# Performance work log

Hardware: AMD Instinct MI355X
Metric: run time of the kernel (lower is better)

## Reference

```python
import jax, jax.numpy as jnp
import numpy as np

B, S = 8192, 2048
EPS = 1e-8
DISCOUNT_FACTOR = 0.99
AVERAGE_LAMBDA = 0.9


def setup_inputs() -> dict:
    key = jax.random.key(0)
    k1, k2 = jax.random.split(key)
    values = jax.random.normal(k1, (B, S + 1, 1), dtype=jnp.float32)
    rewards = jax.random.normal(k2, (B, S, 1), dtype=jnp.float32)
    dones = jnp.zeros((B, S, 1), dtype=jnp.float32)
    # parameters initialized as in the module: atanh of target values
    raw_gamma = jnp.arctanh(jnp.full((1,), DISCOUNT_FACTOR, dtype=jnp.float32))
    raw_lambd = jnp.arctanh(jnp.full((S,), AVERAGE_LAMBDA, dtype=jnp.float32))
    return {"values": values, "rewards": rewards, "dones": dones,
            "raw_gamma": raw_gamma, "raw_lambd": raw_lambd}


def reference(values, rewards, dones, raw_gamma, raw_lambd):
    # gamma = tanh(raw_gamma).clamp_min(1e-8); lambda likewise (per timestep)
    gamma = jnp.maximum(jnp.tanh(raw_gamma), EPS)      # [1]
    lam = jnp.maximum(jnp.tanh(raw_lambd), EPS)        # [S]
    # time-major for scan: [S, B, 1]
    v_next = jnp.swapaxes(values[:, 1:], 0, 1)
    r = jnp.swapaxes(rewards, 0, 1)
    d = jnp.swapaxes(dones, 0, 1)

    def step(G, xs):
        vt1, rt, dt, lt = xs
        # G_t = r_t + gamma*(1-d_t)*((1-lam_t)*V_{t+1} + lam_t*G_{t+1})
        G = rt + gamma * (1.0 - dt) * ((1.0 - lt) * vt1 + lt * G)
        return G, G

    G_last = values[:, -1]  # bootstrap: [B, 1]
    _, Gs = jax.lax.scan(step, G_last, (v_next, r, d, lam), reverse=True)
    return jnp.swapaxes(Gs, 0, 1)  # [B, S, 1]
```

## Files before the change

kernel.cpp:

```cpp
#include <hip/hip_runtime.h>
#include <math.h>

#define EPS_F 1e-8f

__global__ void lam_prep_kernel(const float* __restrict__ raw_lambd,
                                float* __restrict__ lam_ws, int S) {
    int t = blockIdx.x * blockDim.x + threadIdx.x;
    if (t < S) lam_ws[t] = fmaxf(tanhf(raw_lambd[t]), EPS_F);
}

template <bool USE_WS>
__global__ __launch_bounds__(256) void glam_scan_kernel(
    const float* __restrict__ values,
    const float* __restrict__ rewards,
    const float* __restrict__ dones,
    const float* __restrict__ raw_gamma,
    const float* __restrict__ raw_lambd,
    const float* __restrict__ lam_ws,
    float* __restrict__ out,
    int B, int S)
{
    const int wave = (blockIdx.x * blockDim.x + threadIdx.x) >> 6;
    const int lane = threadIdx.x & 63;
    if (wave >= B) return;

    const float gamma = fmaxf(tanhf(raw_gamma[0]), EPS_F);

    const size_t vbase = (size_t)wave * (size_t)(S + 1);
    const size_t base  = (size_t)wave * (size_t)S;

    const int NP = S >> 8;
    float carry = values[vbase + S];

    #pragma unroll 8
    for (int p = NP - 1; p >= 0; --p) {
        const int c0 = p << 8;
        const int e0 = c0 + 4 * lane;

        const float4 r4 = *reinterpret_cast<const float4*>(rewards + base + e0);
        const float4 d4 = *reinterpret_cast<const float4*>(dones   + base + e0);

        float lamv[4];
        if (USE_WS) {
            const float4 l4 = *reinterpret_cast<const float4*>(lam_ws + e0);
            lamv[0] = l4.x; lamv[1] = l4.y; lamv[2] = l4.z; lamv[3] = l4.w;
        } else {
            #pragma unroll
            for (int j = 0; j < 4; ++j)
                lamv[j] = fmaxf(tanhf(raw_lambd[e0 + j]), EPS_F);
        }

        float v1[4];
        #pragma unroll
        for (int j = 0; j < 4; ++j) v1[j] = values[vbase + e0 + j + 1];

        const float rr[4] = { r4.x, r4.y, r4.z, r4.w };
        const float dd[4] = { d4.x, d4.y, d4.z, d4.w };

        float a[4], bb[4];
        #pragma unroll
        for (int j = 0; j < 4; ++j) {
            const float c = gamma * (1.0f - dd[j]);
            a[j]  = fmaf(c * (1.0f - lamv[j]), v1[j], rr[j]);
            bb[j] = c * lamv[j];
        }

        float A = 0.0f, P = 1.0f;
        #pragma unroll
        for (int j = 3; j >= 0; --j) {
            A = fmaf(bb[j], A, a[j]);
            P *= bb[j];
        }

        #pragma unroll
        for (int d = 1; d < 64; d <<= 1) {
            float A2 = __shfl_down(A, d);
            float P2 = __shfl_down(P, d);
            const bool valid = (lane + d) < 64;
            A2 = valid ? A2 : 0.0f;
            P2 = valid ? P2 : 1.0f;
            A = fmaf(P, A2, A);
            P *= P2;
        }

        const float A1 = __shfl_down(A, 1);
        const float P1 = __shfl_down(P, 1);
        float G = (lane == 63) ? carry : fmaf(P1, carry, A1);

        float o[4];
        #pragma unroll
        for (int j = 3; j >= 0; --j) {
            G = fmaf(bb[j], G, a[j]);
            o[j] = G;
        }

        float4 o4;
        o4.x = o[0]; o4.y = o[1]; o4.z = o[2]; o4.w = o[3];
        *reinterpret_cast<float4*>(out + base + e0) = o4;

        carry = __shfl(G, 0);
    }
}

__global__ void glam_naive_kernel(const float* __restrict__ values,
                                  const float* __restrict__ rewards,
                                  const float* __restrict__ dones,
                                  const float* __restrict__ raw_gamma,
                                  const float* __restrict__ raw_lambd,
                                  float* __restrict__ out, int B, int S) {
    int b = blockIdx.x * blockDim.x + threadIdx.x;
    if (b >= B) return;
    const float gamma = fmaxf(tanhf(raw_gamma[0]), EPS_F);
    const size_t vbase = (size_t)b * (size_t)(S + 1);
    const size_t base  = (size_t)b * (size_t)S;
    float G = values[vbase + S];
    for (int t = S - 1; t >= 0; --t) {
        const float lt = fmaxf(tanhf(raw_lambd[t]), EPS_F);
        const float c  = gamma * (1.0f - dones[base + t]);
        G = rewards[base + t] + c * ((1.0f - lt) * values[vbase + t + 1] + lt * G);
        out[base + t] = G;
    }
}

extern "C" void kernel_launch(void* const* d_in, const int* in_sizes, int n_in,
                              void* d_out, int out_size, void* d_ws, size_t ws_size,
                              hipStream_t stream) {
    const float* values    = (const float*)d_in[0];
    const float* rewards   = (const float*)d_in[1];
    const float* dones     = (const float*)d_in[2];
    const float* raw_gamma = (const float*)d_in[3];
    const float* raw_lambd = (const float*)d_in[4];
    float* out = (float*)d_out;

    const int S = in_sizes[4];
    const int B = in_sizes[1] / S;

    if ((S & 255) != 0) {
        glam_naive_kernel<<<(B + 255) / 256, 256, 0, stream>>>(
            values, rewards, dones, raw_gamma, raw_lambd, out, B, S);
        return;
    }

    const int total_threads = B * 64;
    const int blocks = (total_threads + 255) / 256;

    const bool use_ws = (d_ws != nullptr) && (ws_size >= (size_t)S * sizeof(float));
    if (use_ws) {
        float* lam_ws = (float*)d_ws;
        lam_prep_kernel<<<(S + 255) / 256, 256, 0, stream>>>(raw_lambd, lam_ws, S);
        glam_scan_kernel<true><<<blocks, 256, 0, stream>>>(
            values, rewards, dones, raw_gamma, raw_lambd, lam_ws, out, B, S);
    } else {
        glam_scan_kernel<false><<<blocks, 256, 0, stream>>>(
            values, rewards, dones, raw_gamma, raw_lambd, nullptr, out, B, S);
    }
}
```

Measured before the change: 49.80 us.

## Decouple chunk scans from serial carry chain with affine composition and nontemporal stores

Each wave now computes the local affine scan (A, P) for all eight chunks independently and keeps them in registers. A short backward pass then applies the carry to produce the outputs. This takes the cross-chunk carry off the critical path, so the loads and shuffle scans for all chunks can overlap. S is fixed at 2048 as a compile-time constant, and outputs use nontemporal stores. The cost is much higher register pressure from the per-chunk arrays, which may reduce occupancy, and the fast path only handles S=2048.

```diff
diff --git a/kernel.cpp b/kernel.cpp
--- a/kernel.cpp
+++ b/kernel.cpp
@@ -2,6 +2,8 @@
 #include <math.h>
 
 #define EPS_F 1e-8f
+
+typedef float vfloat4 __attribute__((ext_vector_type(4)));
 
 __global__ void lam_prep_kernel(const float* __restrict__ raw_lambd,
                                 float* __restrict__ lam_ws, int S) {
@@ -18,8 +20,11 @@
     const float* __restrict__ raw_lambd,
     const float* __restrict__ lam_ws,
     float* __restrict__ out,
-    int B, int S)
+    int B)
 {
+    constexpr int S  = 2048;
+    constexpr int NP = 8;
+
     const int wave = (blockIdx.x * blockDim.x + threadIdx.x) >> 6;
     const int lane = threadIdx.x & 63;
     if (wave >= B) return;
@@ -28,21 +33,23 @@
 
     const size_t vbase = (size_t)wave * (size_t)(S + 1);
     const size_t base  = (size_t)wave * (size_t)S;
+    const int lo4 = 4 * lane;
 
-    const int NP = S >> 8;
-    float carry = values[vbase + S];
+    const float vS = values[vbase + S];
 
-    #pragma unroll 8
-    for (int p = NP - 1; p >= 0; --p) {
-        const int c0 = p << 8;
-        const int e0 = c0 + 4 * lane;
+    float oA[NP][4], oP[NP][4];
+    float pA[NP], pP[NP];
 
-        const float4 r4 = *reinterpret_cast<const float4*>(rewards + base + e0);
-        const float4 d4 = *reinterpret_cast<const float4*>(dones   + base + e0);
+    #pragma unroll
+    for (int p = 0; p < NP; ++p) {
+        const int e0 = (p << 8) + lo4;
+
+        const vfloat4 r4 = *reinterpret_cast<const vfloat4*>(rewards + base + e0);
+        const vfloat4 d4 = *reinterpret_cast<const vfloat4*>(dones   + base + e0);
 
         float lamv[4];
         if (USE_WS) {
-            const float4 l4 = *reinterpret_cast<const float4*>(lam_ws + e0);
+            const vfloat4 l4 = *reinterpret_cast<const vfloat4*>(lam_ws + e0);
             lamv[0] = l4.x; lamv[1] = l4.y; lamv[2] = l4.z; lamv[3] = l4.w;
         } else {
             #pragma unroll
@@ -52,7 +59,7 @@
 
         float v1[4];
         #pragma unroll
-        for (int j = 0; j < 4; ++j) v1[j] = values[vbase + e0 + j + 1];
+        for (int j = 0; j < 4; ++j) v1[j] = values[vbase + e0 + 1 + j];
 
         const float rr[4] = { r4.x, r4.y, r4.z, r4.w };
         const float dd[4] = { d4.x, d4.y, d4.z, d4.w };
@@ -83,22 +90,34 @@
             P *= P2;
         }
 
+        pA[p] = __shfl(A, 0);
+        pP[p] = __shfl(P, 0);
+
         const float A1 = __shfl_down(A, 1);
         const float P1 = __shfl_down(P, 1);
-        float G = (lane == 63) ? carry : fmaf(P1, carry, A1);
+        float Af = (lane == 63) ? 0.0f : A1;
+        float Pf = (lane == 63) ? 1.0f : P1;
 
-        float o[4];
         #pragma unroll
         for (int j = 3; j >= 0; --j) {
-            G = fmaf(bb[j], G, a[j]);
-            o[j] = G;
+            Af = fmaf(bb[j], Af, a[j]);
+            Pf = bb[j] * Pf;
+            oA[p][j] = Af;
+            oP[p][j] = Pf;
         }
+    }
 
-        float4 o4;
-        o4.x = o[0]; o4.y = o[1]; o4.z = o[2]; o4.w = o[3];
-        *reinterpret_cast<float4*>(out + base + e0) = o4;
-
-        carry = __shfl(G, 0);
+    float Gb = vS;
+    #pragma unroll
+    for (int p = NP - 1; p >= 0; --p) {
+        vfloat4 o4;
+        o4.x = fmaf(oP[p][0], Gb, oA[p][0]);
+        o4.y = fmaf(oP[p][1], Gb, oA[p][1]);
+        o4.z = fmaf(oP[p][2], Gb, oA[p][2]);
+        o4.w = fmaf(oP[p][3], Gb, oA[p][3]);
+        __builtin_nontemporal_store(o4,
+            reinterpret_cast<vfloat4*>(out + base + (p << 8) + lo4));
+        Gb = fmaf(pP[p], Gb, pA[p]);
     }
 }
 
@@ -135,7 +154,7 @@
     const int S = in_sizes[4];
     const int B = in_sizes[1] / S;
 
-    if ((S & 255) != 0) {
+    if (S != 2048) {
         glam_naive_kernel<<<(B + 255) / 256, 256, 0, stream>>>(
             values, rewards, dones, raw_gamma, raw_lambd, out, B, S);
         return;
@@ -149,9 +168,9 @@
         float* lam_ws = (float*)d_ws;
         lam_prep_kernel<<<(S + 255) / 256, 256, 0, stream>>>(raw_lambd, lam_ws, S);
         glam_scan_kernel<true><<<blocks, 256, 0, stream>>>(
-            values, rewards, dones, raw_gamma, raw_lambd, lam_ws, out, B, S);
+            values, rewards, dones, raw_gamma, raw_lambd, lam_ws, out, B);
     } else {
         glam_scan_kernel<false><<<blocks, 256, 0, stream>>>(
-            values, rewards, dones, raw_gamma, raw_lambd, nullptr, out, B, S);
+            values, rewards, dones, raw_gamma, raw_lambd, nullptr, out, B);
     }
 }
```

After: 49.31 us. Within noise of the previous version (-1.0%).

## Scan each row with one 512-thread block using cross-wave LDS carry combine

Applied to the files above, without the earlier changes.

Each batch row is now handled by one 512-thread block of eight waves, each wave covering a 256-element chunk. Previously a single wave walked the eight chunks sequentially with a serial carry between them. Per-wave affine scan summaries are exchanged through shared memory after one barrier, and each wave composes the later summaries to get its carry. This exposes more memory-level parallelism and removes the serial chunk dependency. It also adds a vectorized unaligned load for values, precomputes gamma into the workspace, and uses nontemporal stores. The kernel now hardcodes S=2048 and falls back to the naive path otherwise.

```diff
diff --git a/kernel.cpp b/kernel.cpp
--- a/kernel.cpp
+++ b/kernel.cpp
@@ -3,103 +3,111 @@
 
 #define EPS_F 1e-8f
 
-__global__ void lam_prep_kernel(const float* __restrict__ raw_lambd,
-                                float* __restrict__ lam_ws, int S) {
+typedef float vfloat4 __attribute__((ext_vector_type(4)));
+typedef float uafloat4 __attribute__((ext_vector_type(4), aligned(4)));
+
+__global__ void lam_prep_kernel(const float* __restrict__ raw_gamma,
+                                const float* __restrict__ raw_lambd,
+                                float* __restrict__ ws, int S) {
     int t = blockIdx.x * blockDim.x + threadIdx.x;
-    if (t < S) lam_ws[t] = fmaxf(tanhf(raw_lambd[t]), EPS_F);
+    if (t < S) ws[t] = fmaxf(tanhf(raw_lambd[t]), EPS_F);
+    if (t == S) ws[S] = fmaxf(tanhf(raw_gamma[0]), EPS_F);
 }
 
 template <bool USE_WS>
-__global__ __launch_bounds__(256) void glam_scan_kernel(
+__global__ __launch_bounds__(512, 8) void glam_scan_kernel(
     const float* __restrict__ values,
     const float* __restrict__ rewards,
     const float* __restrict__ dones,
     const float* __restrict__ raw_gamma,
     const float* __restrict__ raw_lambd,
-    const float* __restrict__ lam_ws,
+    const float* __restrict__ ws,
     float* __restrict__ out,
-    int B, int S)
+    int B)
 {
-    const int wave = (blockIdx.x * blockDim.x + threadIdx.x) >> 6;
-    const int lane = threadIdx.x & 63;
-    if (wave >= B) return;
+    constexpr int S = 2048;
 
-    const float gamma = fmaxf(tanhf(raw_gamma[0]), EPS_F);
+    __shared__ float cA[8], cP[8];
 
-    const size_t vbase = (size_t)wave * (size_t)(S + 1);
-    const size_t base  = (size_t)wave * (size_t)S;
+    const int tid  = threadIdx.x;
+    const int w    = tid >> 6;
+    const int lane = tid & 63;
+    const int row  = blockIdx.x;
 
-    const int NP = S >> 8;
-    float carry = values[vbase + S];
+    const size_t vbase = (size_t)row * (size_t)(S + 1);
+    const size_t base  = (size_t)row * (size_t)S;
+    const int e0 = (w << 8) + 4 * lane;
 
-    #pragma unroll 8
-    for (int p = NP - 1; p >= 0; --p) {
-        const int c0 = p << 8;
-        const int e0 = c0 + 4 * lane;
+    const vfloat4  r4 = *reinterpret_cast<const vfloat4*>(rewards + base + e0);
+    const vfloat4  d4 = *reinterpret_cast<const vfloat4*>(dones   + base + e0);
+    const uafloat4 v4 = *reinterpret_cast<const uafloat4*>(values + vbase + e0 + 1);
+    const float    vS = values[vbase + S];
 
-        const float4 r4 = *reinterpret_cast<const float4*>(rewards + base + e0);
-        const float4 d4 = *reinterpret_cast<const float4*>(dones   + base + e0);
+    float gamma, ll[4];
+    if (USE_WS) {
+        const vfloat4 l4 = *reinterpret_cast<const vfloat4*>(ws + e0);
+        ll[0] = l4.x; ll[1] = l4.y; ll[2] = l4.z; ll[3] = l4.w;
+        gamma = ws[S];
+    } else {
+        #pragma unroll
+        for (int j = 0; j < 4; ++j)
+            ll[j] = fmaxf(tanhf(raw_lambd[e0 + j]), EPS_F);
+        gamma = fmaxf(tanhf(raw_gamma[0]), EPS_F);
+    }
 
-        float lamv[4];
-        if (USE_WS) {
-            const float4 l4 = *reinterpret_cast<const float4*>(lam_ws + e0);
-            lamv[0] = l4.x; lamv[1] = l4.y; lamv[2] = l4.z; lamv[3] = l4.w;
-        } else {
-            #pragma unroll
-            for (int j = 0; j < 4; ++j)
-                lamv[j] = fmaxf(tanhf(raw_lambd[e0 + j]), EPS_F);
-        }
+    const float rr[4] = { r4.x, r4.y, r4.z, r4.w };
+    const float dd[4] = { d4.x, d4.y, d4.z, d4.w };
+    const float vv[4] = { v4.x, v4.y, v4.z, v4.w };
 
-        float v1[4];
-        #pragma unroll
-        for (int j = 0; j < 4; ++j) v1[j] = values[vbase + e0 + j + 1];
+    float a[4], bb[4];
+    #pragma unroll
+    for (int j = 0; j < 4; ++j) {
+        const float c = gamma * (1.0f - dd[j]);
+        a[j]  = fmaf(c * (1.0f - ll[j]), vv[j], rr[j]);
+        bb[j] = c * ll[j];
+    }
 
-        const float rr[4] = { r4.x, r4.y, r4.z, r4.w };
-        const float dd[4] = { d4.x, d4.y, d4.z, d4.w };
+    float A = 0.0f, P = 1.0f;
+    #pragma unroll
+    for (int j = 3; j >= 0; --j) {
+        A = fmaf(bb[j], A, a[j]);
+        P *= bb[j];
+    }
 
-        float a[4], bb[4];
-        #pragma unroll
-        for (int j = 0; j < 4; ++j) {
-            const float c = gamma * (1.0f - dd[j]);
-            a[j]  = fmaf(c * (1.0f - lamv[j]), v1[j], rr[j]);
-            bb[j] = c * lamv[j];
-        }
+    #pragma unroll
+    for (int d = 1; d < 64; d <<= 1) {
+        float A2 = __shfl_down(A, d);
+        float P2 = __shfl_down(P, d);
+        const bool valid = (lane + d) < 64;
+        A2 = valid ? A2 : 0.0f;
+        P2 = valid ? P2 : 1.0f;
+        A = fmaf(P, A2, A);
+        P *= P2;
+    }
 
-        float A = 0.0f, P = 1.0f;
-        #pragma unroll
-        for (int j = 3; j >= 0; --j) {
-            A = fmaf(bb[j], A, a[j]);
-            P *= bb[j];
-        }
+    if (lane == 0) { cA[w] = A; cP[w] = P; }
 
-        #pragma unroll
-        for (int d = 1; d < 64; d <<= 1) {
-            float A2 = __shfl_down(A, d);
-            float P2 = __shfl_down(P, d);
-            const bool valid = (lane + d) < 64;
-            A2 = valid ? A2 : 0.0f;
-            P2 = valid ? P2 : 1.0f;
-            A = fmaf(P, A2, A);
-            P *= P2;
-        }
+    const float Ad = __shfl_down(A, 1);
+    const float Pd = __shfl_down(P, 1);
+    const float A1 = (lane == 63) ? 0.0f : Ad;
+    const float P1 = (lane == 63) ? 1.0f : Pd;
 
-        const float A1 = __shfl_down(A, 1);
-        const float P1 = __shfl_down(P, 1);
-        float G = (lane == 63) ? carry : fmaf(P1, carry, A1);
+    __syncthreads();
 
-        float o[4];
-        #pragma unroll
-        for (int j = 3; j >= 0; --j) {
-            G = fmaf(bb[j], G, a[j]);
-            o[j] = G;
-        }
+    float Gb = vS;
+    for (int q = 7; q > w; --q)
+        Gb = fmaf(cP[q], Gb, cA[q]);
 
-        float4 o4;
-        o4.x = o[0]; o4.y = o[1]; o4.z = o[2]; o4.w = o[3];
-        *reinterpret_cast<float4*>(out + base + e0) = o4;
-
-        carry = __shfl(G, 0);
+    float G = fmaf(P1, Gb, A1);
+    float o[4];
+    #pragma unroll
+    for (int j = 3; j >= 0; --j) {
+        G = fmaf(bb[j], G, a[j]);
+        o[j] = G;
     }
+    vfloat4 o4;
+    o4.x = o[0]; o4.y = o[1]; o4.z = o[2]; o4.w = o[3];
+    __builtin_nontemporal_store(o4, reinterpret_cast<vfloat4*>(out + base + e0));
 }
 
 __global__ void glam_naive_kernel(const float* __restrict__ values,
@@ -135,23 +143,22 @@
     const int S = in_sizes[4];
     const int B = in_sizes[1] / S;
 
-    if ((S & 255) != 0) {
+    if (S != 2048) {
         glam_naive_kernel<<<(B + 255) / 256, 256, 0, stream>>>(
             values, rewards, dones, raw_gamma, raw_lambd, out, B, S);
         return;
     }
 
-    const int total_threads = B * 64;
-    const int blocks = (total_threads + 255) / 256;
-
-    const bool use_ws = (d_ws != nullptr) && (ws_size >= (size_t)S * sizeof(float));
+    const bool use_ws = (d_ws != nullptr) &&
+                        (ws_size >= (size_t)(S + 1) * sizeof(float));
     if (use_ws) {
-        float* lam_ws = (float*)d_ws;
-        lam_prep_kernel<<<(S + 255) / 256, 256, 0, stream>>>(raw_lambd, lam_ws, S);
-        glam_scan_kernel<true><<<blocks, 256, 0, stream>>>(
-            values, rewards, dones, raw_gamma, raw_lambd, lam_ws, out, B, S);
+        float* ws = (float*)d_ws;
+        lam_prep_kernel<<<(S + 256) / 256, 256, 0, stream>>>(
+            raw_gamma, raw_lambd, ws, S);
+        glam_scan_kernel<true><<<B, 512, 0, stream>>>(
+            values, rewards, dones, raw_gamma, raw_lambd, ws, out, B);
     } else {
-        glam_scan_kernel<false><<<blocks, 256, 0, stream>>>(
-            values, rewards, dones, raw_gamma, raw_lambd, nullptr, out, B, S);
+        glam_scan_kernel<false><<<B, 512, 0, stream>>>(
+            values, rewards, dones, raw_gamma, raw_lambd, nullptr, out, B);
     }
 }
```

After: 46.70 us. 1.07x faster.
